# Optimization experiments

Hardware: AMD Instinct MI355X
Metric: run time of the kernel (lower is better)

Reference implementation:

```python
import jax, jax.numpy as jnp
import numpy as np

COLOR_SIZE = 8
FILTERS = 128
L = 256 * 256 * 3  # flattened sequence length
EPS = 1e-12  # tf.math.l2_normalize epsilon


def setup_inputs() -> dict:
    key = jax.random.key(0)
    k1, k2, k3, k4, k5, k6 = jax.random.split(key, 6)
    example = jax.random.randint(k1, (4, 256, 256, 3), 0, COLOR_SIZE, dtype=jnp.int32)
    W_in = jax.random.normal(k2, (1, FILTERS), dtype=jnp.float32) * 0.05
    b_in = jnp.zeros((FILTERS,), dtype=jnp.float32)
    pos = jax.random.normal(k3, (L, FILTERS), dtype=jnp.float32) * 0.05
    W_final = jax.random.normal(k4, (FILTERS, COLOR_SIZE), dtype=jnp.float32) * 0.05
    b_final = jnp.zeros((COLOR_SIZE,), dtype=jnp.float32)
    return {"example": example, "W_in": W_in, "b_in": b_in, "pos": pos,
            "W_final": W_final, "b_final": b_final}


def reference(example, W_in, b_in, pos, W_final, b_final):
    B = example.shape[0]
    # cast + rescale to [-1, 1) (applied twice in the original code)
    x = example.astype(jnp.float32) / COLOR_SIZE * 2.0 - 1.0
    x = x.reshape(B, L, 1)
    x = x * 2.0 - 1.0
    # layer 0: Dense(1->F) + positional encoding + relu
    x = x * W_in[0] + b_in + pos  # [B, L, F]
    x = jax.nn.relu(x)
    # causal cumsum over sequence, then l2-normalize feature dim
    s = jnp.cumsum(x, axis=-2)  # [B, L, F]
    x = s * jax.lax.rsqrt(jnp.maximum(jnp.sum(s * s, axis=-1, keepdims=True), EPS))
    # final Dense(F->color_size)
    x = jnp.einsum('blf,fc->blc', x, W_final) + b_final
    return x.reshape(B, 256, 256, 3, COLOR_SIZE)
```

## Files before the change

### kernel.cpp

```cpp
#include <hip/hip_runtime.h>
#include <hip/hip_fp16.h>

#define BB   4
#define FF   128
#define CC   8
#define LSEQ 196608
#define NCH  2048
#define CL   96
#define TL   16
#define NT   6
#define NSEG 32
#define SEGL 64

typedef _Float16 half8 __attribute__((ext_vector_type(8)));
typedef float    f32x4 __attribute__((ext_vector_type(4)));

__global__ __launch_bounds__(64) void k_chunksum(
    const int* __restrict__ ex, const float* __restrict__ W_in,
    const float* __restrict__ b_in, const float* __restrict__ pos,
    float* __restrict__ csum)
{
    __shared__ float xv[BB][CL];
    const int ch = blockIdx.x;
    const int t  = threadIdx.x;
    const int l0 = ch * CL;
    #pragma unroll
    for (int b = 0; b < BB; ++b)
        for (int i = t; i < CL; i += 64)
            xv[b][i] = (float)ex[(size_t)b * LSEQ + l0 + i] * 0.5f - 3.0f;
    __syncthreads();

    const float2 w  = *(const float2*)&W_in[2 * t];
    const float2 bb = *(const float2*)&b_in[2 * t];
    float2 s[BB];
    #pragma unroll
    for (int b = 0; b < BB; ++b) { s[b].x = 0.f; s[b].y = 0.f; }
    const float* pp = pos + (size_t)l0 * FF + 2 * t;
    #pragma unroll 4
    for (int l = 0; l < CL; ++l) {
        float2 p = *(const float2*)pp; pp += FF;
        float px = p.x + bb.x, py = p.y + bb.y;
        #pragma unroll
        for (int b = 0; b < BB; ++b) {
            float x = xv[b][l];
            s[b].x += fmaxf(fmaf(x, w.x, px), 0.f);
            s[b].y += fmaxf(fmaf(x, w.y, py), 0.f);
        }
    }
    #pragma unroll
    for (int b = 0; b < BB; ++b)
        *(float2*)&csum[((size_t)b * NCH + ch) * FF + 2 * t] = s[b];
}

__global__ __launch_bounds__(128) void k_segsum(
    const float* __restrict__ csum, float* __restrict__ segT)
{
    const int seg = blockIdx.x, b = blockIdx.y, f = threadIdx.x;
    const float* p = csum + ((size_t)b * NCH + (size_t)seg * SEGL) * FF + f;
    float a = 0.f;
    #pragma unroll 8
    for (int i = 0; i < SEGL; ++i) a += p[(size_t)i * FF];
    segT[((size_t)b * NSEG + seg) * FF + f] = a;
}

__global__ __launch_bounds__(128) void k_segscan(float* __restrict__ segT)
{
    const int b = blockIdx.x, f = threadIdx.x;
    float acc = 0.f;
    for (int s = 0; s < NSEG; ++s) {
        size_t idx = ((size_t)b * NSEG + s) * FF + f;
        float v = segT[idx];
        segT[idx] = acc;
        acc += v;
    }
}

__global__ __launch_bounds__(128) void k_chscan(
    float* __restrict__ csum, const float* __restrict__ segT)
{
    const int seg = blockIdx.x, b = blockIdx.y, f = threadIdx.x;
    float acc = segT[((size_t)b * NSEG + seg) * FF + f];
    float* p = csum + ((size_t)b * NCH + (size_t)seg * SEGL) * FF + f;
    #pragma unroll 8
    for (int i = 0; i < SEGL; ++i) {
        float v = p[(size_t)i * FF];
        p[(size_t)i * FF] = acc;
        acc += v;
    }
}

__global__ __launch_bounds__(256, 4) void k_final(
    const int* __restrict__ ex, const float* __restrict__ W_in,
    const float* __restrict__ b_in, const float* __restrict__ pos,
    const float* __restrict__ Wf, const float* __restrict__ bfin,
    const float* __restrict__ csum, float* __restrict__ out)
{
    __shared__ __align__(16) __half stile[BB][TL][FF];
    __shared__ float xv[BB][CL];

    const int ch   = blockIdx.x;
    const int l0   = ch * CL;
    const int t    = threadIdx.x;
    const int b    = t >> 6;
    const int lane = t & 63;
    const int lo   = lane & 15;
    const int hi   = lane >> 4;

    for (int i = lane; i < CL; i += 64)
        xv[b][i] = (float)ex[(size_t)b * LSEQ + l0 + i] * 0.5f - 3.0f;

    half8 wfrag[4];
    float bfc = (lo < CC) ? bfin[lo] : 0.f;
    #pragma unroll
    for (int kk = 0; kk < 4; ++kk) {
        #pragma unroll
        for (int j = 0; j < 8; ++j) {
            int k = kk * 32 + hi * 8 + j;
            float wv = (lo < CC) ? Wf[k * CC + lo] : 0.f;
            wfrag[kk][j] = (_Float16)wv;
        }
    }

    const float2 w  = *(const float2*)&W_in[2 * lane];
    const float2 bb = *(const float2*)&b_in[2 * lane];
    float2 s = *(const float2*)&csum[((size_t)b * NCH + ch) * FF + 2 * lane];

    char* sbase = (char*)&stile[b][0][0];
    const int ra0 = lo * 256 + ((hi * 16) ^ ((lo & 7) << 4));
    const int wa  = 4 * lane;

    for (int tile = 0; tile < NT; ++tile) {
        const float* pp = pos + (size_t)(l0 + tile * TL) * FF + 2 * lane;
        #pragma unroll
        for (int l = 0; l < TL; ++l) {
            float2 p = *(const float2*)pp; pp += FF;
            float x = xv[b][tile * TL + l];
            s.x = fmaxf(fmaf(x, w.x, p.x + bb.x), 0.f) + s.x;
            s.y = fmaxf(fmaf(x, w.y, p.y + bb.y), 0.f) + s.y;
            __half2 h = __float22half2_rn(make_float2(s.x, s.y));
            *(__half2*)(sbase + l * 256 + (wa ^ ((l & 7) << 4))) = h;
        }

        f32x4 y  = {0.f, 0.f, 0.f, 0.f};
        f32x4 c2 = {0.f, 0.f, 0.f, 0.f};
        #pragma unroll
        for (int kk = 0; kk < 4; ++kk) {
            half8 a = *(half8*)(sbase + (ra0 ^ (kk << 6)));
            y  = __builtin_amdgcn_mfma_f32_16x16x32_f16(a, wfrag[kk], y, 0, 0, 0);
            c2 = __builtin_amdgcn_mfma_f32_16x16x32_f16(a, a,        c2, 0, 0, 0);
        }

        int i0 = lo - 4 * hi;
        float qd = c2[0];
        qd = (i0 == 1) ? c2[1] : qd;
        qd = (i0 == 2) ? c2[2] : qd;
        qd = (i0 == 3) ? c2[3] : qd;
        float rr = rsqrtf(fmaxf(qd, 1e-12f));
        int sl = 80 * hi;
        float r0 = __int_as_float(__builtin_amdgcn_ds_bpermute(sl,      __float_as_int(rr)));
        float r1 = __int_as_float(__builtin_amdgcn_ds_bpermute(sl + 4,  __float_as_int(rr)));
        float r2 = __int_as_float(__builtin_amdgcn_ds_bpermute(sl + 8,  __float_as_int(rr)));
        float r3 = __int_as_float(__builtin_amdgcn_ds_bpermute(sl + 12, __float_as_int(rr)));

        if (lo < CC) {
            float* op = out + (((size_t)b * LSEQ) + l0 + tile * TL) * CC + lo;
            op[(4 * hi + 0) * CC] = fmaf(y[0], r0, bfc);
            op[(4 * hi + 1) * CC] = fmaf(y[1], r1, bfc);
            op[(4 * hi + 2) * CC] = fmaf(y[2], r2, bfc);
            op[(4 * hi + 3) * CC] = fmaf(y[3], r3, bfc);
        }
    }
}

extern "C" void kernel_launch(void* const* d_in, const int* in_sizes, int n_in,
                              void* d_out, int out_size, void* d_ws, size_t ws_size,
                              hipStream_t stream) {
    const int*   ex   = (const int*)d_in[0];
    const float* W_in = (const float*)d_in[1];
    const float* b_in = (const float*)d_in[2];
    const float* pos  = (const float*)d_in[3];
    const float* Wf   = (const float*)d_in[4];
    const float* bf   = (const float*)d_in[5];
    float* out  = (float*)d_out;
    float* csum = (float*)d_ws;
    float* segT = csum + (size_t)BB * NCH * FF;

    k_chunksum<<<NCH, 64, 0, stream>>>(ex, W_in, b_in, pos, csum);
    k_segsum  <<<dim3(NSEG, BB), 128, 0, stream>>>(csum, segT);
    k_segscan <<<BB, 128, 0, stream>>>(segT);
    k_chscan  <<<dim3(NSEG, BB), 128, 0, stream>>>(csum, segT);
    k_final   <<<NCH, 256, 0, stream>>>(ex, W_in, b_in, pos, Wf, bf, csum, out);
}
```

Before: 69.59 us.

## Merge chunk scan into one serial kernel and coalesce output stores via LDS

Replaces the three-kernel segmented scan (segment sums, segment scan, chunk scan) with a single kernel that uses one block of 64 threads per batch, each thread walking all 2048 chunks serially with float2 accesses. In the final kernel, per-tile outputs are staged in a small shared buffer so that 16 lanes write full 32-byte rows with vector stores. It also partially unrolls the tile loop. This removes two launches and the extra segT buffer, but leaves the scan with only 4 blocks and a long serial chain of dependent memory round-trips.

```diff
diff --git a/kernel.cpp b/kernel.cpp
--- a/kernel.cpp
+++ b/kernel.cpp
@@ -9,8 +9,6 @@
 #define CL   96
 #define TL   16
 #define NT   6
-#define NSEG 32
-#define SEGL 64
 
 typedef _Float16 half8 __attribute__((ext_vector_type(8)));
 typedef float    f32x4 __attribute__((ext_vector_type(4)));
@@ -52,40 +50,17 @@
         *(float2*)&csum[((size_t)b * NCH + ch) * FF + 2 * t] = s[b];
 }
 
-__global__ __launch_bounds__(128) void k_segsum(
-    const float* __restrict__ csum, float* __restrict__ segT)
+__global__ __launch_bounds__(64) void k_scan2(float* __restrict__ csum)
 {
-    const int seg = blockIdx.x, b = blockIdx.y, f = threadIdx.x;
-    const float* p = csum + ((size_t)b * NCH + (size_t)seg * SEGL) * FF + f;
-    float a = 0.f;
-    #pragma unroll 8
-    for (int i = 0; i < SEGL; ++i) a += p[(size_t)i * FF];
-    segT[((size_t)b * NSEG + seg) * FF + f] = a;
-}
-
-__global__ __launch_bounds__(128) void k_segscan(float* __restrict__ segT)
-{
-    const int b = blockIdx.x, f = threadIdx.x;
-    float acc = 0.f;
-    for (int s = 0; s < NSEG; ++s) {
-        size_t idx = ((size_t)b * NSEG + s) * FF + f;
-        float v = segT[idx];
-        segT[idx] = acc;
-        acc += v;
-    }
-}
-
-__global__ __launch_bounds__(128) void k_chscan(
-    float* __restrict__ csum, const float* __restrict__ segT)
-{
-    const int seg = blockIdx.x, b = blockIdx.y, f = threadIdx.x;
-    float acc = segT[((size_t)b * NSEG + seg) * FF + f];
-    float* p = csum + ((size_t)b * NCH + (size_t)seg * SEGL) * FF + f;
-    #pragma unroll 8
-    for (int i = 0; i < SEGL; ++i) {
-        float v = p[(size_t)i * FF];
-        p[(size_t)i * FF] = acc;
-        acc += v;
+    const int b = blockIdx.x, t = threadIdx.x;
+    float2 acc = {0.f, 0.f};
+    float* p = csum + (size_t)b * NCH * FF + 2 * t;
+    #pragma unroll 4
+    for (int ch = 0; ch < NCH; ++ch) {
+        float2 v = *(float2*)p;
+        *(float2*)p = acc;
+        acc.x += v.x; acc.y += v.y;
+        p += FF;
     }
 }
 
@@ -96,6 +71,7 @@
     const float* __restrict__ csum, float* __restrict__ out)
 {
     __shared__ __align__(16) __half stile[BB][TL][FF];
+    __shared__ __align__(16) float  tbuf[BB][TL][CC];
     __shared__ float xv[BB][CL];
 
     const int ch   = blockIdx.x;
@@ -129,6 +105,7 @@
     const int ra0 = lo * 256 + ((hi * 16) ^ ((lo & 7) << 4));
     const int wa  = 4 * lane;
 
+    #pragma unroll 2
     for (int tile = 0; tile < NT; ++tile) {
         const float* pp = pos + (size_t)(l0 + tile * TL) * FF + 2 * lane;
         #pragma unroll
@@ -163,11 +140,17 @@
         float r3 = __int_as_float(__builtin_amdgcn_ds_bpermute(sl + 12, __float_as_int(rr)));
 
         if (lo < CC) {
-            float* op = out + (((size_t)b * LSEQ) + l0 + tile * TL) * CC + lo;
-            op[(4 * hi + 0) * CC] = fmaf(y[0], r0, bfc);
-            op[(4 * hi + 1) * CC] = fmaf(y[1], r1, bfc);
-            op[(4 * hi + 2) * CC] = fmaf(y[2], r2, bfc);
-            op[(4 * hi + 3) * CC] = fmaf(y[3], r3, bfc);
+            tbuf[b][4 * hi + 0][lo] = fmaf(y[0], r0, bfc);
+            tbuf[b][4 * hi + 1][lo] = fmaf(y[1], r1, bfc);
+            tbuf[b][4 * hi + 2][lo] = fmaf(y[2], r2, bfc);
+            tbuf[b][4 * hi + 3][lo] = fmaf(y[3], r3, bfc);
+        }
+        if (lane < TL) {
+            const f32x4* tp = (const f32x4*)&tbuf[b][lane][0];
+            f32x4 v0 = tp[0], v1 = tp[1];
+            float* op = out + (((size_t)b * LSEQ) + l0 + tile * TL + lane) * CC;
+            *(f32x4*)op       = v0;
+            *(f32x4*)(op + 4) = v1;
         }
     }
 }
@@ -183,11 +166,8 @@
     const float* bf   = (const float*)d_in[5];
     float* out  = (float*)d_out;
     float* csum = (float*)d_ws;
-    float* segT = csum + (size_t)BB * NCH * FF;
 
     k_chunksum<<<NCH, 64, 0, stream>>>(ex, W_in, b_in, pos, csum);
-    k_segsum  <<<dim3(NSEG, BB), 128, 0, stream>>>(csum, segT);
-    k_segscan <<<BB, 128, 0, stream>>>(segT);
-    k_chscan  <<<dim3(NSEG, BB), 128, 0, stream>>>(csum, segT);
+    k_scan2   <<<BB, 64, 0, stream>>>(csum);
     k_final   <<<NCH, 256, 0, stream>>>(ex, W_in, b_in, pos, Wf, bf, csum, out);
 }
```

Result: slower. 200.8 us (+188.5%).
